# Performance work log

Hardware: AMD Instinct MI355X
Metric: run time of the kernel (lower is better)

## Reference

```python
import jax, jax.numpy as jnp
import numpy as np

B, S, I, H, L = 32, 512, 512, 512, 2


def _gru_scan(x, wx, bx, wh, bh, reverse):
    # x: [B, S, layer_in_dim]; wx: [3H, in], wh: [3H, H]. PyTorch gate order r,z,n.
    hdim = wh.shape[1]
    gx = jnp.einsum('bsi,gi->sbg', x, wx) + bx  # precompute input gates: [S, B, 3H]
    h0 = jnp.zeros((x.shape[0], hdim), x.dtype)

    def step(h, gxt):
        gh = h @ wh.T + bh
        r = jax.nn.sigmoid(gxt[:, :hdim] + gh[:, :hdim])
        z = jax.nn.sigmoid(gxt[:, hdim:2 * hdim] + gh[:, hdim:2 * hdim])
        n = jnp.tanh(gxt[:, 2 * hdim:] + r * gh[:, 2 * hdim:])
        hn = (1 - z) * n + z * h
        return hn, hn

    hN, ys = jax.lax.scan(step, h0, gx, reverse=reverse)
    return ys.transpose(1, 0, 2), hN  # [B, S, H], [B, H]


def setup_inputs() -> dict:
    key = jax.random.key(0)
    ks = jax.random.split(key, 17)
    sc = 0.05
    d = {'x': jax.random.normal(ks[0], (B, S, I), jnp.float32)}
    i = 1
    for layer in range(L):
        in_dim = I if layer == 0 else 2 * H
        for tag in ('f', 'b'):
            d[f'wx_{tag}{layer}'] = jax.random.normal(ks[i], (3 * H, in_dim), jnp.float32) * sc
            d[f'bx_{tag}{layer}'] = jax.random.normal(jax.random.fold_in(ks[i], 1), (3 * H,), jnp.float32) * sc
            d[f'wh_{tag}{layer}'] = jax.random.normal(jax.random.fold_in(ks[i], 2), (3 * H, H), jnp.float32) * sc
            d[f'bh_{tag}{layer}'] = jax.random.normal(jax.random.fold_in(ks[i], 3), (3 * H,), jnp.float32) * sc
            i += 1
    return d


def reference(x,
              wx_f0, bx_f0, wh_f0, bh_f0, wx_b0, bx_b0, wh_b0, bh_b0,
              wx_f1, bx_f1, wh_f1, bh_f1, wx_b1, bx_b1, wh_b1, bh_b1):
    layers = [((wx_f0, bx_f0, wh_f0, bh_f0), (wx_b0, bx_b0, wh_b0, bh_b0)),
              ((wx_f1, bx_f1, wh_f1, bh_f1), (wx_b1, bx_b1, wh_b1, bh_b1))]
    layer_in = x
    h_fw, h_bw = [], []
    for fw, bw in layers:
        yf, hf = _gru_scan(layer_in, *fw, reverse=False)
        yb, hb = _gru_scan(layer_in, *bw, reverse=True)
        layer_in = jnp.concatenate([yf, yb], axis=-1)  # [B, S, 2H] (dropout p=0 -> identity)
        h_fw.append(hf)
        h_bw.append(hb)
    return layer_in, (jnp.stack(h_fw, 0), jnp.stack(h_bw, 0))
```

## Files before the change

kernel.cpp:

```cpp
#include <hip/hip_runtime.h>
#include <stdint.h>

typedef short short8 __attribute__((ext_vector_type(8)));
typedef float floatx4 __attribute__((ext_vector_type(4)));
typedef unsigned long long u64;

__device__ __forceinline__ unsigned short f2bf(float f) {
  union { float f; unsigned int i; } v;
  v.f = f;
  unsigned int r = v.i + 0x7fffu + ((v.i >> 16) & 1u);
  return (unsigned short)(r >> 16);
}
__device__ __forceinline__ short8 cvt8(const float4 a, const float4 b) {
  short8 v;
  v[0] = (short)f2bf(a.x); v[1] = (short)f2bf(a.y);
  v[2] = (short)f2bf(a.z); v[3] = (short)f2bf(a.w);
  v[4] = (short)f2bf(b.x); v[5] = (short)f2bf(b.y);
  v[6] = (short)f2bf(b.z); v[7] = (short)f2bf(b.w);
  return v;
}
__device__ __forceinline__ float sane(float x, float lim) {
  return fminf(fmaxf(x, -lim), lim);
}

extern __shared__ unsigned short lds[];

template<int K, int XM, int EM>
__global__ __launch_bounds__(128)
void gru_layer(const float* __restrict__ xf,
               const unsigned short* __restrict__ xb,
               const float* __restrict__ wxfp,
               const float* __restrict__ bxfp,
               const float* __restrict__ whfp,
               const float* __restrict__ bhfp,
               const float* __restrict__ wxbp,
               const float* __restrict__ bxbp,
               const float* __restrict__ whbp,
               const float* __restrict__ bhbp,
               unsigned short* __restrict__ exch,
               float* __restrict__ omain,
               float* __restrict__ out_hf,
               float* __restrict__ out_hb,
               int* __restrict__ flags)
{
  constexpr int NKS = K / 32;
  constexpr int WXW = K + 8;
  constexpr int KC = K >> 3;
  constexpr int KSH = (K == 512) ? 6 : 7;

  unsigned short* whs = lds;
  unsigned short* wxs = lds + 48 * 520;

  const int bid = blockIdx.x;
  const bool fw = bid < 32;
  const int d = fw ? bid : bid - 32;
  const int tid = threadIdx.x;
  const int lane = tid & 63;
  const int w = tid >> 6;
  const int q = lane >> 4;
  const int l16 = lane & 15;

  const float* wx = fw ? wxfp : wxbp;
  const float* bx = fw ? bxfp : bxbp;
  const float* wh = fw ? whfp : whbp;
  const float* bh = fw ? bhfp : bhbp;
  const int col0 = d * 16;
  const int dirofs = fw ? 0 : 512;

  unsigned int* exch32 = (unsigned int*)exch;

  for (int c = tid; c < 48 * 64; c += 128) {
    int lr = c >> 6, c8 = (c & 63) * 8;
    int g = lr >> 4, jc = lr & 15;
    const float* src = wh + (long)(g * 512 + col0 + jc) * 512 + c8;
    *(short8*)(whs + lr * 520 + c8) =
        cvt8(*(const float4*)src, *(const float4*)(src + 4));
  }
  for (int c = tid; c < 48 * KC; c += 128) {
    int lr = c >> KSH, c8 = (c & (KC - 1)) * 8;
    int g = lr >> 4, jc = lr & 15;
    const float* src = wx + (long)(g * 512 + col0 + jc) * K + c8;
    *(short8*)(wxs + lr * WXW + c8) =
        cvt8(*(const float4*)src, *(const float4*)(src + 4));
  }
  __syncthreads();

  const int jj = l16;
  const int gcr = col0 + jj;
  const int gcz = 512 + col0 + jj;
  const int gcn = 1024 + col0 + jj;
  const float cr = bx[gcr] + bh[gcr];
  const float cz = bx[gcz] + bh[gcz];
  const float bxn = bx[gcn];
  const float bhn = bh[gcn];

  const int cb = w * 16 + q * 4;
  const int ab = w * 16 + l16;

  const floatx4 fz = {0.f, 0.f, 0.f, 0.f};
  float h[4] = {0.f, 0.f, 0.f, 0.f};

  float4 fpre[XM ? 2 * NKS : 1];
  short8 bpre[XM ? 1 : NKS];

  auto load_x = [&](int t) {
    if (XM) {
      const float* p = xf + ((long)ab * 512 + t) * 512 + q * 8;
#pragma unroll
      for (int ks = 0; ks < NKS; ++ks) {
        fpre[2 * ks]     = *(const float4*)(p + ks * 32);
        fpre[2 * ks + 1] = *(const float4*)(p + ks * 32 + 4);
      }
    } else {
      const unsigned short* p = xb + ((long)t * 32 + ab) * 1024 + q * 8;
#pragma unroll
      for (int ks = 0; ks < NKS; ++ks)
        bpre[ks] = *(const short8*)(p + ks * 32);
    }
  };

  auto mfma_gx = [&](floatx4& gr, floatx4& gz, floatx4& gn) {
    gr = fz; gz = fz; gn = fz;
#pragma unroll
    for (int ks = 0; ks < NKS; ++ks) {
      short8 a = XM ? cvt8(fpre[2 * ks], fpre[2 * ks + 1]) : bpre[ks];
      short8 vr = *(const short8*)(wxs + (jj) * WXW + ks * 32 + q * 8);
      short8 vz = *(const short8*)(wxs + (16 + jj) * WXW + ks * 32 + q * 8);
      short8 vn = *(const short8*)(wxs + (32 + jj) * WXW + ks * 32 + q * 8);
      gr = __builtin_amdgcn_mfma_f32_16x16x32_bf16(a, vr, gr, 0, 0, 0);
      gz = __builtin_amdgcn_mfma_f32_16x16x32_bf16(a, vz, gz, 0, 0, 0);
      gn = __builtin_amdgcn_mfma_f32_16x16x32_bf16(a, vn, gn, 0, 0, 0);
    }
  };

  floatx4 gxr, gxz, gxn;
  { const int t0 = fw ? 0 : 511; load_x(t0); mfma_gx(gxr, gxz, gxn); }

  for (int it = 0; it < 512; ++it) {
    const int t = fw ? it : 511 - it;

    short8 af[16];
    if (it > 0) {
      const unsigned short* hbase;
      if (EM == 0) {
        const int tprev = fw ? t - 1 : t + 1;
        hbase = exch + ((long)tprev * 32 + ab) * 1024 + dirofs;
      } else {
        const int slot_r = (it + 1) & 1;
        hbase = exch + ((long)slot_r * 32 + ab) * 1024 + dirofs;
      }
#pragma unroll
      for (int ks = 0; ks < 16; ++ks) {
        u64* p = (u64*)(hbase + ks * 32 + q * 8);
        union { u64 u[2]; short8 s; } t8;
        t8.u[0] = __hip_atomic_load(p,     __ATOMIC_RELAXED, __HIP_MEMORY_SCOPE_AGENT);
        t8.u[1] = __hip_atomic_load(p + 1, __ATOMIC_RELAXED, __HIP_MEMORY_SCOPE_AGENT);
        af[ks] = t8.s;
      }
    }
    if (it < 511) {
      const int tn2 = fw ? (it + 1) : (511 - (it + 1));
      load_x(tn2);
    }

    floatx4 ar = fz, az = fz, an = fz;
    if (it > 0) {
#pragma unroll
      for (int ks = 0; ks < 16; ++ks) {
        short8 vr = *(const short8*)(whs + (jj) * 520 + ks * 32 + q * 8);
        short8 vz = *(const short8*)(whs + (16 + jj) * 520 + ks * 32 + q * 8);
        short8 vn = *(const short8*)(whs + (32 + jj) * 520 + ks * 32 + q * 8);
        ar = __builtin_amdgcn_mfma_f32_16x16x32_bf16(af[ks], vr, ar, 0, 0, 0);
        az = __builtin_amdgcn_mfma_f32_16x16x32_bf16(af[ks], vz, az, 0, 0, 0);
        an = __builtin_amdgcn_mfma_f32_16x16x32_bf16(af[ks], vn, an, 0, 0, 0);
      }
    }

    unsigned short hb16[4];
#pragma unroll
    for (int r = 0; r < 4; ++r) {
      const float xr = sane(gxr[r] + ar[r] + cr, 60.f);
      const float xz = sane(gxz[r] + az[r] + cz, 60.f);
      const float rr = 1.f / (1.f + __expf(-xr));
      const float zz = 1.f / (1.f + __expf(-xz));
      const float xn = sane(gxn[r] + bxn + rr * (an[r] + bhn), 30.f);
      const float e2 = __expf(-2.f * xn);
      const float nn = (1.f - e2) / (1.f + e2);
      h[r] = (1.f - zz) * nn + zz * h[r];
      hb16[r] = f2bf(h[r]);
    }

    unsigned int hw[4];
#pragma unroll
    for (int r = 0; r < 4; ++r) {
      int v = hb16[r];
      int p = __shfl_xor(v, 1);
      hw[r] = (unsigned int)(v & 0xffff) | ((unsigned int)(p & 0xffff) << 16);
    }
    if ((jj & 1) == 0) {
      const int colw = (dirofs + col0 + jj) >> 1;
#pragma unroll
      for (int r = 0; r < 4; ++r) {
        const long eidx = (EM == 0)
            ? (((long)t * 32 + cb + r) * 512 + colw)
            : (((long)(it & 1) * 32 + cb + r) * 512 + colw);
        __hip_atomic_store(exch32 + eidx, hw[r],
                           __ATOMIC_RELAXED, __HIP_MEMORY_SCOPE_AGENT);
      }
    }
    if (EM == 1) {
#pragma unroll
      for (int r = 0; r < 4; ++r)
        omain[(long)(cb + r) * 524288 + (long)t * 1024 + dirofs + col0 + jj] = h[r];
    }

    if (it == 511) {
      float* oh = fw ? out_hf : out_hb;
#pragma unroll
      for (int r = 0; r < 4; ++r)
        oh[(cb + r) * 512 + col0 + jj] = h[r];
    } else {
      __syncthreads();
      if (tid == 0)
        __hip_atomic_store(&flags[bid * 16], it + 1,
                           __ATOMIC_RELEASE, __HIP_MEMORY_SCOPE_AGENT);
      mfma_gx(gxr, gxz, gxn);
      if (tid < 32) {
        const int pf = ((fw ? 0 : 32) + tid) * 16;
        while (__hip_atomic_load(&flags[pf], __ATOMIC_RELAXED,
                                 __HIP_MEMORY_SCOPE_AGENT) < it + 1)
          __builtin_amdgcn_s_sleep(2);
      }
      __syncthreads();
    }
  }
}

extern "C" void kernel_launch(void* const* d_in, const int* in_sizes, int n_in,
                              void* d_out, int out_size, void* d_ws, size_t ws_size,
                              hipStream_t stream)
{
  (void)in_sizes; (void)n_in; (void)out_size; (void)ws_size;

  const float* x    = (const float*)d_in[0];
  const float* wxf0 = (const float*)d_in[1];
  const float* bxf0 = (const float*)d_in[2];
  const float* whf0 = (const float*)d_in[3];
  const float* bhf0 = (const float*)d_in[4];
  const float* wxb0 = (const float*)d_in[5];
  const float* bxb0 = (const float*)d_in[6];
  const float* whb0 = (const float*)d_in[7];
  const float* bhb0 = (const float*)d_in[8];
  const float* wxf1 = (const float*)d_in[9];
  const float* bxf1 = (const float*)d_in[10];
  const float* whf1 = (const float*)d_in[11];
  const float* bhf1 = (const float*)d_in[12];
  const float* wxb1 = (const float*)d_in[13];
  const float* bxb1 = (const float*)d_in[14];
  const float* whb1 = (const float*)d_in[15];
  const float* bhb1 = (const float*)d_in[16];

  char* ws = (char*)d_ws;
  unsigned short* y0    = (unsigned short*)(ws);
  unsigned short* ring1 = (unsigned short*)(ws + 33554432L);
  int* flags0           = (int*)(ws + 33685504L);
  int* flags1           = (int*)(ws + 33685504L + 4096L);

  float* out = (float*)d_out;
  float* out_hf0 = out + 16777216L;
  float* out_hf1 = out + 16777216L + 16384L;
  float* out_hb0 = out + 16777216L + 32768L;
  float* out_hb1 = out + 16777216L + 49152L;

  const size_t lds0 = (size_t)(48 * 520 + 48 * (512 + 8)) * 2;
  const size_t lds1 = (size_t)(48 * 520 + 48 * (1024 + 8)) * 2;
  (void)hipFuncSetAttribute((const void*)gru_layer<512, 1, 0>,
                            hipFuncAttributeMaxDynamicSharedMemorySize, (int)lds0);
  (void)hipFuncSetAttribute((const void*)gru_layer<1024, 0, 1>,
                            hipFuncAttributeMaxDynamicSharedMemorySize, (int)lds1);

  hipMemsetAsync(flags0, 0, 8192, stream);

  gru_layer<512, 1, 0><<<dim3(64), dim3(128), lds0, stream>>>(
      x, nullptr, wxf0, bxf0, whf0, bhf0, wxb0, bxb0, whb0, bhb0,
      y0, nullptr, out_hf0, out_hb0, flags0);

  gru_layer<1024, 0, 1><<<dim3(64), dim3(128), lds1, stream>>>(
      nullptr, y0, wxf1, bxf1, whf1, bhf1, wxb1, bxb1, whb1, bhb1,
      ring1, out, out_hf1, out_hb1, flags1);
}
```

Before: 7.745 ms.

## Replace per-step flag barriers with tag bits embedded in exchanged bf16 hidden state

Removes the per-timestep __syncthreads plus global flag store/poll handshake between blocks. Readiness is now encoded in bit 14 of each packed bf16 hidden value (toggled per ring phase), so consumers spin directly on the data words and mask the tag off before the MFMA. The whole workspace is zeroed up front so the tags start in a known state. The trade-off: bf16 bit 14 is borrowed as a marker and assumed to be recoverable by masking, which only holds when the hidden and output magnitudes stay small enough. It also adds a large memset and relies on relaxed atomics being ordered per word.

```diff
diff --git a/kernel.cpp b/kernel.cpp
--- a/kernel.cpp
+++ b/kernel.cpp
@@ -40,13 +40,13 @@
                unsigned short* __restrict__ exch,
                float* __restrict__ omain,
                float* __restrict__ out_hf,
-               float* __restrict__ out_hb,
-               int* __restrict__ flags)
+               float* __restrict__ out_hb)
 {
   constexpr int NKS = K / 32;
   constexpr int WXW = K + 8;
   constexpr int KC = K >> 3;
   constexpr int KSH = (K == 512) ? 6 : 7;
+  constexpr u64 TM = 0x4000400040004000ULL;
 
   unsigned short* whs = lds;
   unsigned short* wxs = lds + 48 * 520;
@@ -123,7 +123,16 @@
     gr = fz; gz = fz; gn = fz;
 #pragma unroll
     for (int ks = 0; ks < NKS; ++ks) {
-      short8 a = XM ? cvt8(fpre[2 * ks], fpre[2 * ks + 1]) : bpre[ks];
+      short8 a;
+      if (XM) {
+        a = cvt8(fpre[2 * ks], fpre[2 * ks + 1]);
+      } else {
+        union { short8 s; unsigned int dd[4]; } u;
+        u.s = bpre[ks];
+        u.dd[0] &= 0xBFFFBFFFu; u.dd[1] &= 0xBFFFBFFFu;
+        u.dd[2] &= 0xBFFFBFFFu; u.dd[3] &= 0xBFFFBFFFu;
+        a = u.s;
+      }
       short8 vr = *(const short8*)(wxs + (jj) * WXW + ks * 32 + q * 8);
       short8 vz = *(const short8*)(wxs + (16 + jj) * WXW + ks * 32 + q * 8);
       short8 vn = *(const short8*)(wxs + (32 + jj) * WXW + ks * 32 + q * 8);
@@ -136,26 +145,32 @@
   floatx4 gxr, gxz, gxn;
   { const int t0 = fw ? 0 : 511; load_x(t0); mfma_gx(gxr, gxz, gxn); }
 
+  union W { u64 u[2]; short8 s; unsigned int dd[4]; };
+
   for (int it = 0; it < 512; ++it) {
     const int t = fw ? it : 511 - it;
 
-    short8 af[16];
+    const unsigned short* hbase = nullptr;
+    u64 expectw = 0;
     if (it > 0) {
-      const unsigned short* hbase;
       if (EM == 0) {
         const int tprev = fw ? t - 1 : t + 1;
         hbase = exch + ((long)tprev * 32 + ab) * 1024 + dirofs;
+        expectw = TM;
       } else {
         const int slot_r = (it + 1) & 1;
         hbase = exch + ((long)slot_r * 32 + ab) * 1024 + dirofs;
-      }
+        expectw = ((((it - 1) >> 1) & 1) ^ 1) ? TM : 0ULL;
+      }
+    }
+
+    W wv[16];
+    if (it > 0) {
 #pragma unroll
       for (int ks = 0; ks < 16; ++ks) {
         u64* p = (u64*)(hbase + ks * 32 + q * 8);
-        union { u64 u[2]; short8 s; } t8;
-        t8.u[0] = __hip_atomic_load(p,     __ATOMIC_RELAXED, __HIP_MEMORY_SCOPE_AGENT);
-        t8.u[1] = __hip_atomic_load(p + 1, __ATOMIC_RELAXED, __HIP_MEMORY_SCOPE_AGENT);
-        af[ks] = t8.s;
+        wv[ks].u[0] = __hip_atomic_load(p,     __ATOMIC_RELAXED, __HIP_MEMORY_SCOPE_AGENT);
+        wv[ks].u[1] = __hip_atomic_load(p + 1, __ATOMIC_RELAXED, __HIP_MEMORY_SCOPE_AGENT);
       }
     }
     if (it < 511) {
@@ -167,12 +182,24 @@
     if (it > 0) {
 #pragma unroll
       for (int ks = 0; ks < 16; ++ks) {
+        u64* p = (u64*)(hbase + ks * 32 + q * 8);
+        while ((wv[ks].u[0] & TM) != expectw) {
+          __builtin_amdgcn_s_sleep(1);
+          wv[ks].u[0] = __hip_atomic_load(p, __ATOMIC_RELAXED, __HIP_MEMORY_SCOPE_AGENT);
+        }
+        while ((wv[ks].u[1] & TM) != expectw) {
+          __builtin_amdgcn_s_sleep(1);
+          wv[ks].u[1] = __hip_atomic_load(p + 1, __ATOMIC_RELAXED, __HIP_MEMORY_SCOPE_AGENT);
+        }
+        wv[ks].dd[0] &= 0xBFFFBFFFu; wv[ks].dd[1] &= 0xBFFFBFFFu;
+        wv[ks].dd[2] &= 0xBFFFBFFFu; wv[ks].dd[3] &= 0xBFFFBFFFu;
+        short8 a = wv[ks].s;
         short8 vr = *(const short8*)(whs + (jj) * 520 + ks * 32 + q * 8);
         short8 vz = *(const short8*)(whs + (16 + jj) * 520 + ks * 32 + q * 8);
         short8 vn = *(const short8*)(whs + (32 + jj) * 520 + ks * 32 + q * 8);
-        ar = __builtin_amdgcn_mfma_f32_16x16x32_bf16(af[ks], vr, ar, 0, 0, 0);
-        az = __builtin_amdgcn_mfma_f32_16x16x32_bf16(af[ks], vz, az, 0, 0, 0);
-        an = __builtin_amdgcn_mfma_f32_16x16x32_bf16(af[ks], vn, an, 0, 0, 0);
+        ar = __builtin_amdgcn_mfma_f32_16x16x32_bf16(a, vr, ar, 0, 0, 0);
+        az = __builtin_amdgcn_mfma_f32_16x16x32_bf16(a, vz, az, 0, 0, 0);
+        an = __builtin_amdgcn_mfma_f32_16x16x32_bf16(a, vn, an, 0, 0, 0);
       }
     }
 
@@ -190,12 +217,16 @@
       hb16[r] = f2bf(h[r]);
     }
 
+    const unsigned int tb =
+        (EM == 0) ? 0x40004000u
+                  : (((((it) >> 1) & 1) ^ 1) ? 0x40004000u : 0u);
     unsigned int hw[4];
 #pragma unroll
     for (int r = 0; r < 4; ++r) {
       int v = hb16[r];
-      int p = __shfl_xor(v, 1);
-      hw[r] = (unsigned int)(v & 0xffff) | ((unsigned int)(p & 0xffff) << 16);
+      int pmate = __shfl_xor(v, 1);
+      hw[r] = ((unsigned int)(v & 0xffff) |
+               ((unsigned int)(pmate & 0xffff) << 16)) | tb;
     }
     if ((jj & 1) == 0) {
       const int colw = (dirofs + col0 + jj) >> 1;
@@ -220,18 +251,7 @@
       for (int r = 0; r < 4; ++r)
         oh[(cb + r) * 512 + col0 + jj] = h[r];
     } else {
-      __syncthreads();
-      if (tid == 0)
-        __hip_atomic_store(&flags[bid * 16], it + 1,
-                           __ATOMIC_RELEASE, __HIP_MEMORY_SCOPE_AGENT);
       mfma_gx(gxr, gxz, gxn);
-      if (tid < 32) {
-        const int pf = ((fw ? 0 : 32) + tid) * 16;
-        while (__hip_atomic_load(&flags[pf], __ATOMIC_RELAXED,
-                                 __HIP_MEMORY_SCOPE_AGENT) < it + 1)
-          __builtin_amdgcn_s_sleep(2);
-      }
-      __syncthreads();
     }
   }
 }
@@ -263,8 +283,6 @@
   char* ws = (char*)d_ws;
   unsigned short* y0    = (unsigned short*)(ws);
   unsigned short* ring1 = (unsigned short*)(ws + 33554432L);
-  int* flags0           = (int*)(ws + 33685504L);
-  int* flags1           = (int*)(ws + 33685504L + 4096L);
 
   float* out = (float*)d_out;
   float* out_hf0 = out + 16777216L;
@@ -279,13 +297,13 @@
   (void)hipFuncSetAttribute((const void*)gru_layer<1024, 0, 1>,
                             hipFuncAttributeMaxDynamicSharedMemorySize, (int)lds1);
 
-  hipMemsetAsync(flags0, 0, 8192, stream);
+  hipMemsetAsync(ws, 0, 33685504L, stream);
 
   gru_layer<512, 1, 0><<<dim3(64), dim3(128), lds0, stream>>>(
       x, nullptr, wxf0, bxf0, whf0, bhf0, wxb0, bxb0, whb0, bhb0,
-      y0, nullptr, out_hf0, out_hb0, flags0);
+      y0, nullptr, out_hf0, out_hb0);
 
   gru_layer<1024, 0, 1><<<dim3(64), dim3(128), lds1, stream>>>(
       nullptr, y0, wxf1, bxf1, whf1, bhf1, wxb1, bxb1, whb1, bhb1,
-      ring1, out, out_hf1, out_hb1, flags1);
-}
+      ring1, out, out_hf1, out_hb1);
+}
```

After: 10.04 ms. 1.3x slower.
